# Kernel tuning notes

Measured on AMD Instinct MI355X. Metric: run time of the kernel, lower is better.

The kernel has to match this reference:

```python
import jax, jax.numpy as jnp
import numpy as np

HEADS, KV_HEADS, HEAD_DIM = 16, 4, 128
WINDOW, ROPE_THETA, EPS = 512, 10000.0, 1e-6


def _rms_norm(x, w):
    # Gemma RMSNorm: float32 compute, scale = 1 + w
    xf = x.astype(jnp.float32)
    y = xf * jax.lax.rsqrt(jnp.mean(xf * xf, axis=-1, keepdims=True) + EPS)
    return (y * (1.0 + w.astype(jnp.float32))).astype(x.dtype)


def _rope_cos_sin(T, dtype):
    inv_freq = 1.0 / ROPE_THETA ** (jnp.arange(0, HEAD_DIM, 2, dtype=jnp.float32) / HEAD_DIM)
    pos = jnp.arange(T, dtype=jnp.float32)
    freqs = pos[:, None] * inv_freq[None, :]          # [T, Dh/2]
    emb = jnp.concatenate([freqs, freqs], axis=-1)    # [T, Dh]
    return emb.astype(dtype), emb  # cos/sin applied below


def _rotate_half(x):
    x1, x2 = jnp.split(x, 2, axis=-1)
    return jnp.concatenate([-x2, x1], axis=-1)


def setup_inputs() -> dict:
    key = jax.random.key(0)
    ks = jax.random.split(key, 7)
    B, T, D = 2, 2048, 2048
    s = lambda k, shape, fan: jax.random.normal(k, shape, jnp.float32) * (fan ** -0.5)
    return {
        "x": jax.random.normal(ks[0], (B, T, D), jnp.float32),
        "Wq": s(ks[1], (HEADS * HEAD_DIM, D), D),
        "Wk": s(ks[2], (KV_HEADS * HEAD_DIM, D), D),
        "Wv": s(ks[3], (KV_HEADS * HEAD_DIM, D), D),
        "Wo": s(ks[4], (D, HEADS * HEAD_DIM), HEADS * HEAD_DIM),
        "qn_w": jax.random.normal(ks[5], (HEAD_DIM,), jnp.float32) * 0.02,
        "kn_w": jax.random.normal(ks[6], (HEAD_DIM,), jnp.float32) * 0.02,
    }


def reference(x, Wq, Wk, Wv, Wo, qn_w, kn_w):
    B, T, D = x.shape
    H, Hkv, Dh = HEADS, KV_HEADS, HEAD_DIM
    G = H // Hkv

    q = (x @ Wq.T).reshape(B, T, H, Dh).transpose(0, 2, 1, 3)     # [B,H,T,Dh]
    k = (x @ Wk.T).reshape(B, T, Hkv, Dh).transpose(0, 2, 1, 3)   # [B,Hkv,T,Dh]
    v = (x @ Wv.T).reshape(B, T, Hkv, Dh).transpose(0, 2, 1, 3)

    q = _rms_norm(q, qn_w)
    k = _rms_norm(k, kn_w)

    emb_c, emb_f = _rope_cos_sin(T, x.dtype)
    cos = jnp.cos(emb_f).astype(x.dtype)[None, None]  # [1,1,T,Dh]
    sin = jnp.sin(emb_f).astype(x.dtype)[None, None]
    q = q * cos + _rotate_half(q) * sin
    k = k * cos + _rotate_half(k) * sin

    q = q * (Dh ** -0.5)
    qg = q.reshape(B, Hkv, G, T, Dh)

    scores = jnp.einsum('bhgtd,bhkd->bhgtk', qg.astype(jnp.float32), k.astype(jnp.float32))

    dist = jnp.arange(T)[:, None] - jnp.arange(T)[None, :]        # [T,T]
    mask = (dist >= 0) & (dist <= WINDOW)
    scores = jnp.where(mask[None, None, None], scores, jnp.finfo(jnp.float32).min)
    att = jax.nn.softmax(scores, axis=-1).astype(x.dtype)

    ctx = jnp.einsum('bhgtk,bhkd->bhgtd', att, v)                 # [B,Hkv,G,T,Dh]
    out = ctx.reshape(B, H, T, Dh).transpose(0, 2, 1, 3).reshape(B, T, H * Dh)
    return out @ Wo.T
```

## Files before the change

### kernel.cpp

```cpp
#include <hip/hip_runtime.h>
#include <stdint.h>


typedef __attribute__((ext_vector_type(8))) short bf16x8;
typedef __attribute__((ext_vector_type(4))) float f32x4;

typedef __attribute__((address_space(3))) unsigned int lds_u32;
typedef const __attribute__((address_space(1))) unsigned int glb_u32;

__device__ __forceinline__ unsigned short f2bf(float f) {
  unsigned int x = __builtin_bit_cast(unsigned int, f);
  x += 0x7FFFu + ((x >> 16) & 1u);
  return (unsigned short)(x >> 16);
}

__global__ __launch_bounds__(256) void castall(const float* __restrict__ x,
                                               const float* __restrict__ wq,
                                               const float* __restrict__ wk,
                                               const float* __restrict__ wv,
                                               const float* __restrict__ wo,
                                               unsigned short* __restrict__ xb,
                                               unsigned short* __restrict__ wqkvb,
                                               unsigned short* __restrict__ wob) {
  int i = blockIdx.x * 256 + threadIdx.x;
  const float* src;
  unsigned short* dst;
  int off;
  if (i < 2097152)       { src = x;  dst = xb;              off = i; }
  else if (i < 3145728)  { src = wq; dst = wqkvb;           off = i - 2097152; }
  else if (i < 3407872)  { src = wk; dst = wqkvb + 4194304; off = i - 3145728; }
  else if (i < 3670016)  { src = wv; dst = wqkvb + 5242880; off = i - 3407872; }
  else                   { src = wo; dst = wob;             off = i - 3670016; }
  float4 v = ((const float4*)src)[off];
  uint2 o;
  o.x = (unsigned)f2bf(v.x) | ((unsigned)f2bf(v.y) << 16);
  o.y = (unsigned)f2bf(v.z) | ((unsigned)f2bf(v.w) << 16);
  ((uint2*)dst)[off] = o;
}

__global__ __launch_bounds__(256) void rope_tab(float* __restrict__ c,
                                                float* __restrict__ s) {
  int idx = blockIdx.x * 256 + threadIdx.x;
  int t = idx >> 6, i = idx & 63;
  float invf = exp2f(-(float)i * (13.287712379549449f / 64.0f));
  float a = (float)t * invf;
  c[idx] = cosf(a);
  s[idx] = sinf(a);
}

template <int BN>
__global__ __launch_bounds__(512, 2) void gemm256(const unsigned short* __restrict__ A,
                                                  const unsigned short* __restrict__ Bm,
                                                  float* __restrict__ C,
                                                  int N, int K) {
  constexpr int BSL = BN * 128;
  __shared__ uint8_t lds[65536 + 2 * BSL];
  const int tid = threadIdx.x, lane = tid & 63, w = tid >> 6;
  const int wm = w >> 2, wn = w & 3;
  const size_t m0 = (size_t)blockIdx.y * 256, n0 = (size_t)blockIdx.x * BN;
  const int srow = lane >> 3;
  const int schunk = (lane & 7) ^ srow;

  f32x4 acc[8][BN / 64];
#pragma unroll
  for (int i = 0; i < 8; ++i)
#pragma unroll
    for (int j = 0; j < BN / 64; ++j) acc[i][j] = f32x4{0.f, 0.f, 0.f, 0.f};

  const int NT = K >> 6;

  auto stageA = [&](int t, int par) {
    uint8_t* slot = lds + (par << 15);
#pragma unroll
    for (int j = 0; j < 4; ++j) {
      int r0 = (j * 8 + w) * 8;
      const unsigned short* src =
          A + (m0 + r0 + srow) * (size_t)K + t * 64 + schunk * 8;
      __builtin_amdgcn_global_load_lds((glb_u32*)src,
                                       (lds_u32*)(slot + r0 * 128), 16, 0, 0);
    }
  };
  auto stageB = [&](int t, int par) {
    uint8_t* slot = lds + 65536 + par * BSL;
#pragma unroll
    for (int j = 0; j < BN / 64; ++j) {
      int r0 = (j * 8 + w) * 8;
      const unsigned short* src =
          Bm + (n0 + r0 + srow) * (size_t)K + t * 64 + schunk * 8;
      __builtin_amdgcn_global_load_lds((glb_u32*)src,
                                       (lds_u32*)(slot + r0 * 128), 16, 0, 0);
    }
  };
  auto compute = [&](int par, int h) {
    const uint8_t* Asl = lds + (par << 15);
    const uint8_t* Bsl = lds + 65536 + par * BSL;
    bf16x8 af[8], bf[BN / 64];
    const int x7 = lane & 7;
    const int cx = h * 4 + (lane >> 4);
    const int rab = wm * 128 + (lane & 15);
    const int rbb = wn * (BN / 4) + (lane & 15);
#pragma unroll
    for (int mt = 0; mt < 8; ++mt)
      af[mt] = *(const bf16x8*)(Asl + (rab + mt * 16) * 128 + ((cx ^ x7) << 4));
#pragma unroll
    for (int nt = 0; nt < BN / 64; ++nt)
      bf[nt] = *(const bf16x8*)(Bsl + (rbb + nt * 16) * 128 + ((cx ^ x7) << 4));
    __builtin_amdgcn_s_setprio(1);
#pragma unroll
    for (int mt = 0; mt < 8; ++mt)
#pragma unroll
      for (int nt = 0; nt < BN / 64; ++nt)
        acc[mt][nt] = __builtin_amdgcn_mfma_f32_16x16x32_bf16(
            af[mt], bf[nt], acc[mt][nt], 0, 0, 0);
    __builtin_amdgcn_s_setprio(0);
  };

  stageA(0, 0);
  stageB(0, 0);
  for (int t = 0; t < NT - 1; ++t) {
    const int p = t & 1, q = p ^ 1;
    stageA(t + 1, q);
    asm volatile("s_waitcnt vmcnt(4)" ::: "memory");
    __builtin_amdgcn_s_barrier();
    __builtin_amdgcn_sched_barrier(0);
    compute(p, 0);
    stageB(t + 1, q);
    compute(p, 1);
    asm volatile("" ::: "memory");
    __builtin_amdgcn_s_barrier();
    __builtin_amdgcn_sched_barrier(0);
  }
  {
    const int p = (NT - 1) & 1;
    asm volatile("s_waitcnt vmcnt(0)" ::: "memory");
    __builtin_amdgcn_s_barrier();
    __builtin_amdgcn_sched_barrier(0);
    compute(p, 0);
    compute(p, 1);
  }
#pragma unroll
  for (int mt = 0; mt < 8; ++mt)
#pragma unroll
    for (int nt = 0; nt < BN / 64; ++nt) {
      size_t row = m0 + wm * 128 + mt * 16 + (lane >> 4) * 4;
      size_t col = n0 + wn * (BN / 4) + nt * 16 + (lane & 15);
#pragma unroll
      for (int r = 0; r < 4; ++r)
        C[(row + r) * N + col] = acc[mt][nt][r];
    }
}

__global__ __launch_bounds__(256) void eplg(const float* __restrict__ qkv,
                                            const float* __restrict__ qw,
                                            const float* __restrict__ kw,
                                            const float* __restrict__ rc,
                                            const float* __restrict__ rs,
                                            unsigned short* __restrict__ qb,
                                            unsigned short* __restrict__ kb) {
  const int row = blockIdx.x;
  const int t = row & 2047;
  const int lane = threadIdx.x & 63, w = threadIdx.x >> 6;
  const float* base = qkv + (size_t)row * 3072;
  const int d0 = 2 * lane;
  const float c0 = rc[t * 64 + (d0 & 63)];
  const float c1 = rc[t * 64 + ((d0 + 1) & 63)];
  const float s0 = rs[t * 64 + (d0 & 63)];
  const float s1 = rs[t * 64 + ((d0 + 1) & 63)];
  const float sgn = (lane < 32) ? -1.0f : 1.0f;
  const float QS = 0.12751744817f;

#pragma unroll
  for (int hh = 0; hh < 4; ++hh) {
    int h = w * 4 + hh;
    float2 x = *(const float2*)(base + h * 128 + d0);
    float ss = x.x * x.x + x.y * x.y;
#pragma unroll
    for (int m = 1; m < 64; m <<= 1) ss += __shfl_xor(ss, m);
    float r = rsqrtf(ss * (1.0f / 128.0f) + 1e-6f);
    float y0 = x.x * r * (1.0f + qw[d0]);
    float y1 = x.y * r * (1.0f + qw[d0 + 1]);
    float p0 = __shfl_xor(y0, 32);
    float p1 = __shfl_xor(y1, 32);
    float o0 = (y0 * c0 + sgn * p0 * s0) * QS;
    float o1 = (y1 * c1 + sgn * p1 * s1) * QS;
    unsigned int pk = (unsigned)f2bf(o0) | ((unsigned)f2bf(o1) << 16);
    *(unsigned int*)(qb + (size_t)row * 2048 + h * 128 + d0) = pk;
  }
  {
    float2 x = *(const float2*)(base + 2048 + w * 128 + d0);
    float ss = x.x * x.x + x.y * x.y;
#pragma unroll
    for (int m = 1; m < 64; m <<= 1) ss += __shfl_xor(ss, m);
    float r = rsqrtf(ss * (1.0f / 128.0f) + 1e-6f);
    float y0 = x.x * r * (1.0f + kw[d0]);
    float y1 = x.y * r * (1.0f + kw[d0 + 1]);
    float p0 = __shfl_xor(y0, 32);
    float p1 = __shfl_xor(y1, 32);
    float o0 = y0 * c0 + sgn * p0 * s0;
    float o1 = y1 * c1 + sgn * p1 * s1;
    unsigned int pk = (unsigned)f2bf(o0) | ((unsigned)f2bf(o1) << 16);
    *(unsigned int*)(kb + (size_t)row * 512 + w * 128 + d0) = pk;
  }
}

__global__ __launch_bounds__(256) void vtrans(const float* __restrict__ qkvf,
                                              unsigned short* __restrict__ vbt) {
  __shared__ float tile[64][65];
  const int t0 = blockIdx.x * 64;
  const int d0 = blockIdx.y * 64;
  const int b = blockIdx.z;
  const int tid = threadIdx.x;
#pragma unroll
  for (int i = 0; i < 4; ++i) {
    int idx = tid + 256 * i;
    int r = idx >> 4, c4 = idx & 15;
    float4 v = *(const float4*)(qkvf + (size_t)(b * 2048 + t0 + r) * 3072 +
                                2560 + d0 + c4 * 4);
    tile[r][c4 * 4 + 0] = v.x;
    tile[r][c4 * 4 + 1] = v.y;
    tile[r][c4 * 4 + 2] = v.z;
    tile[r][c4 * 4 + 3] = v.w;
  }
  __syncthreads();
  const int dr = tid >> 2, ts = (tid & 3) * 16;
  unsigned short tmp[16];
#pragma unroll
  for (int j = 0; j < 16; ++j) tmp[j] = f2bf(tile[ts + j][dr]);
  uint4* dst = (uint4*)(vbt + (size_t)(b * 512 + d0 + dr) * 2048 + t0 + ts);
  dst[0] = *(uint4*)(tmp);
  dst[1] = *(uint4*)(tmp + 8);
}

__global__ __launch_bounds__(1024) void attn(const unsigned short* __restrict__ qb,
                                             const unsigned short* __restrict__ kb,
                                             const unsigned short* __restrict__ vbt,
                                             unsigned short* __restrict__ ctxb) {
  __shared__ uint8_t Ks[2][64 * 256];
  __shared__ uint8_t Vs[2][128 * 128];
  __shared__ uint8_t Ps[16][16 * 128];
  const int qi = blockIdx.x, kvh = blockIdx.y, b = blockIdx.z;
  const int t0 = qi * 64;
  const int tid = threadIdx.x, lane = tid & 63, w = tid >> 6;
  const int h = kvh * 4 + (w & 3), wq = w >> 2;

  bf16x8 qf[4];
  {
    int qrow = t0 + wq * 16 + (lane & 15);
    const unsigned short* qp =
        qb + (size_t)(b * 2048 + qrow) * 2048 + h * 128 + (lane >> 4) * 8;
#pragma unroll
    for (int kc = 0; kc < 4; ++kc) qf[kc] = *(const bf16x8*)(qp + kc * 32);
  }
  f32x4 of[8];
#pragma unroll
  for (int i = 0; i < 8; ++i) of[i] = f32x4{0.f, 0.f, 0.f, 0.f};
  float m_run[4], l_run[4];
#pragma unroll
  for (int r = 0; r < 4; ++r) { m_run[r] = -1e30f; l_run[r] = 0.0f; }

  int kt0 = t0 - 512; if (kt0 < 0) kt0 = 0;
  const int nt = (t0 + 64 - kt0) >> 6;
  uint8_t* Pw = Ps[w];

  const int krow_s = 4 * w + (lane >> 4);
  const int kchunk_s = (lane & 15) ^ (krow_s & 7);
  const int vrow_s = 8 * w + (lane >> 3);
  const int vchunk_s = (lane & 7) ^ (vrow_s & 7);
  auto stage = [&](int it, int par) {
    int kt = kt0 + (it << 6);
    const unsigned short* ksrc =
        kb + (size_t)(b * 2048 + kt + krow_s) * 512 + kvh * 128 + kchunk_s * 8;
    __builtin_amdgcn_global_load_lds((glb_u32*)ksrc,
                                     (lds_u32*)(&Ks[par][w * 1024]), 16, 0, 0);
    const unsigned short* vsrc =
        vbt + (size_t)(b * 512 + kvh * 128 + vrow_s) * 2048 + kt + vchunk_s * 8;
    __builtin_amdgcn_global_load_lds((glb_u32*)vsrc,
                                     (lds_u32*)(&Vs[par][w * 1024]), 16, 0, 0);
  };

  stage(0, 0);
  for (int it = 0; it < nt; ++it) {
    const int par = it & 1;
    const int kt = kt0 + (it << 6);
    if (it + 1 < nt) {
      stage(it + 1, par ^ 1);
      asm volatile("s_waitcnt vmcnt(2)" ::: "memory");
    } else {
      asm volatile("s_waitcnt vmcnt(0)" ::: "memory");
    }
    __builtin_amdgcn_s_barrier();
    __builtin_amdgcn_sched_barrier(0);

    f32x4 sf[4];
#pragma unroll
    for (int nc = 0; nc < 4; ++nc) {
      f32x4 s = f32x4{0.f, 0.f, 0.f, 0.f};
      int key = nc * 16 + (lane & 15);
#pragma unroll
      for (int kc = 0; kc < 4; ++kc) {
        bf16x8 kf = *(const bf16x8*)(
            Ks[par] + key * 256 + (((lane >> 4) * 16 + kc * 64) ^ ((key & 7) << 4)));
        s = __builtin_amdgcn_mfma_f32_16x16x32_bf16(qf[kc], kf, s, 0, 0, 0);
      }
      sf[nc] = s;
    }
#pragma unroll
    for (int nc = 0; nc < 4; ++nc) {
      int j = kt + nc * 16 + (lane & 15);
#pragma unroll
      for (int r = 0; r < 4; ++r) {
        int tq = t0 + wq * 16 + (lane >> 4) * 4 + r;
        if (!((j <= tq) && (tq - j <= 512))) sf[nc][r] = -1e30f;
      }
    }
    float mx[4];
#pragma unroll
    for (int r = 0; r < 4; ++r) {
      float m = fmaxf(fmaxf(sf[0][r], sf[1][r]), fmaxf(sf[2][r], sf[3][r]));
      m = fmaxf(m, __shfl_xor(m, 1));
      m = fmaxf(m, __shfl_xor(m, 2));
      m = fmaxf(m, __shfl_xor(m, 4));
      m = fmaxf(m, __shfl_xor(m, 8));
      mx[r] = m;
    }
    bool grow = (mx[0] > m_run[0] + 8.0f) | (mx[1] > m_run[1] + 8.0f) |
                (mx[2] > m_run[2] + 8.0f) | (mx[3] > m_run[3] + 8.0f);
    if (__any(grow)) {
      float alpha[4];
#pragma unroll
      for (int r = 0; r < 4; ++r) {
        float mn = fmaxf(m_run[r], mx[r]);
        alpha[r] = exp2f(m_run[r] - mn);
        m_run[r] = mn;
        l_run[r] *= alpha[r];
      }
#pragma unroll
      for (int i = 0; i < 8; ++i)
#pragma unroll
        for (int r = 0; r < 4; ++r) of[i][r] *= alpha[r];
    }
    float l_add[4] = {0.f, 0.f, 0.f, 0.f};
#pragma unroll
    for (int nc = 0; nc < 4; ++nc)
#pragma unroll
      for (int r = 0; r < 4; ++r) {
        float p = exp2f(sf[nc][r] - m_run[r]);
        sf[nc][r] = p;
        l_add[r] += p;
      }
#pragma unroll
    for (int r = 0; r < 4; ++r) {
      float la = l_add[r];
      la += __shfl_xor(la, 1);
      la += __shfl_xor(la, 2);
      la += __shfl_xor(la, 4);
      la += __shfl_xor(la, 8);
      l_run[r] += la;
    }
#pragma unroll
    for (int nc = 0; nc < 4; ++nc) {
      int key = nc * 16 + (lane & 15);
#pragma unroll
      for (int r = 0; r < 4; ++r) {
        int prow = (lane >> 4) * 4 + r;
        *(unsigned short*)(Pw + prow * 128 + ((key * 2) ^ ((prow & 7) << 4))) =
            f2bf(sf[nc][r]);
      }
    }
#pragma unroll
    for (int ks = 0; ks < 2; ++ks) {
      int prow = lane & 15;
      bf16x8 pf = *(const bf16x8*)(
          Pw + prow * 128 + ((ks * 64 + (lane >> 4) * 16) ^ ((prow & 7) << 4)));
#pragma unroll
      for (int nc8 = 0; nc8 < 8; ++nc8) {
        int vrow = nc8 * 16 + (lane & 15);
        bf16x8 vf = *(const bf16x8*)(
            Vs[par] + vrow * 128 + ((ks * 64 + (lane >> 4) * 16) ^ ((vrow & 7) << 4)));
        of[nc8] = __builtin_amdgcn_mfma_f32_16x16x32_bf16(pf, vf, of[nc8], 0, 0, 0);
      }
    }
    asm volatile("" ::: "memory");
    __builtin_amdgcn_s_barrier();
    __builtin_amdgcn_sched_barrier(0);
  }
#pragma unroll
  for (int nc8 = 0; nc8 < 8; ++nc8)
#pragma unroll
    for (int r = 0; r < 4; ++r) {
      int tq = t0 + wq * 16 + (lane >> 4) * 4 + r;
      int col = h * 128 + nc8 * 16 + (lane & 15);
      ctxb[(size_t)(b * 2048 + tq) * 2048 + col] = f2bf(of[nc8][r] / l_run[r]);
    }
}

extern "C" void kernel_launch(void* const* d_in, const int* in_sizes, int n_in,
                              void* d_out, int out_size, void* d_ws, size_t ws_size,
                              hipStream_t stream) {
  const float* x  = (const float*)d_in[0];
  const float* Wq = (const float*)d_in[1];
  const float* Wk = (const float*)d_in[2];
  const float* Wv = (const float*)d_in[3];
  const float* Wo = (const float*)d_in[4];
  const float* qw = (const float*)d_in[5];
  const float* kw = (const float*)d_in[6];

  uint8_t* ws = (uint8_t*)d_ws;
  if (ws_size < 131072000ull) return;
  unsigned short* xb    = (unsigned short*)(ws);
  unsigned short* wqkvb = (unsigned short*)(ws + 16777216);
  unsigned short* wob   = (unsigned short*)(ws + 29360128);
  float*          qkvf  = (float*)(ws + 37748736);
  unsigned short* qb2   = (unsigned short*)(ws + 88080384);
  unsigned short* kb2   = (unsigned short*)(ws + 104857600);
  unsigned short* vbt   = (unsigned short*)(ws + 109051904);
  unsigned short* ctxb  = (unsigned short*)(ws + 113246208);
  float*          ropec = (float*)(ws + 130023424);
  float*          ropes = (float*)(ws + 130547712);

  castall<<<18432, 256, 0, stream>>>(x, Wq, Wk, Wv, Wo, xb, wqkvb, wob);
  rope_tab<<<512, 256, 0, stream>>>(ropec, ropes);
  {
    dim3 g(3072 / 256, 4096 / 256);
    gemm256<256><<<g, 512, 0, stream>>>(xb, wqkvb, qkvf, 3072, 2048);
  }
  eplg<<<4096, 256, 0, stream>>>(qkvf, qw, kw, ropec, ropes, qb2, kb2);
  {
    dim3 g(32, 8, 2);
    vtrans<<<g, 256, 0, stream>>>(qkvf, vbt);
  }
  {
    dim3 g(32, 4, 2);
    attn<<<g, 1024, 0, stream>>>(qb2, kb2, vbt, ctxb);
  }
  {
    dim3 g(2048 / 128, 4096 / 256);
    gemm256<128><<<g, 512, 0, stream>>>(ctxb, wob, (float*)d_out, 2048, 2048);
  }
}
```

Baseline: 285.6 us.

## Add ping-pong pipelined 256x256 GEMM for QKV projection with split-K LDS stages

Adds a new bf16 MFMA GEMM kernel for the QKV projection that splits each 64-wide K tile into two 32-wide LDS slots. It stages loads for upcoming tiles with global_load_lds while computing the current half-tiles, interleaving barriers and raised wave priority around MFMA bursts. It also uses a different LDS swizzle. The aim is to overlap global memory traffic with matrix math and keep the MFMA units busier. The cost is a 128 KB LDS footprint and many barriers per iteration, which may limit occupancy, and the schedule relies on hand-tuned vmcnt counts.

Measured after the change: 285.7 us. Within noise of the previous version (+0.0%).

```diff
diff --git a/kernel.cpp b/kernel.cpp
--- a/kernel.cpp
+++ b/kernel.cpp
@@ -48,6 +48,142 @@
   s[idx] = sinf(a);
 }
 
+__global__ __launch_bounds__(512, 2) void gemm8p(const unsigned short* __restrict__ A,
+                                                 const unsigned short* __restrict__ Bm,
+                                                 float* __restrict__ C,
+                                                 int N, int K) {
+  __shared__ uint8_t lds[131072];
+  const int tid = threadIdx.x, lane = tid & 63, w = tid >> 6;
+  const int wm = w >> 2, wn = w & 3;
+  const size_t m0 = (size_t)blockIdx.y * 256, n0 = (size_t)blockIdx.x * 256;
+  const int s_rl = lane >> 2;
+  const int s_c  = ((lane & 3) + 4 - ((lane >> 3) & 3)) & 3;
+
+  f32x4 acc[8][4];
+#pragma unroll
+  for (int i = 0; i < 8; ++i)
+#pragma unroll
+    for (int j = 0; j < 4; ++j) acc[i][j] = f32x4{0.f, 0.f, 0.f, 0.f};
+
+  auto slot = [&](int par, int op, int ks) -> uint8_t* {
+    return lds + (((par * 2 + op) * 2 + ks) << 14);
+  };
+  auto stage = [&](const unsigned short* P, size_t row0, int t, int ks,
+                   uint8_t* sl) {
+#pragma unroll
+    for (int j = 0; j < 2; ++j) {
+      int seg = j * 8 + w;
+      const unsigned short* src =
+          P + (row0 + seg * 16 + s_rl) * (size_t)K + t * 64 + ks * 32 + s_c * 8;
+      __builtin_amdgcn_global_load_lds((glb_u32*)src,
+                                       (lds_u32*)(sl + seg * 1024), 16, 0, 0);
+    }
+  };
+  auto readA = [&](int par, int ks, int qm, bf16x8* out) {
+    const uint8_t* sl = slot(par, 0, ks);
+#pragma unroll
+    for (int mt = 0; mt < 4; ++mt) {
+      int r = wm * 128 + qm * 64 + mt * 16 + (lane & 15);
+      int c = lane >> 4;
+      out[mt] = *(const bf16x8*)(sl + r * 64 + (((c + ((r >> 1) & 3)) & 3) << 4));
+    }
+  };
+  auto readB = [&](int par, int ks, bf16x8* out) {
+    const uint8_t* sl = slot(par, 1, ks);
+#pragma unroll
+    for (int nt = 0; nt < 4; ++nt) {
+      int r = wn * 64 + nt * 16 + (lane & 15);
+      int c = lane >> 4;
+      out[nt] = *(const bf16x8*)(sl + r * 64 + (((c + ((r >> 1) & 3)) & 3) << 4));
+    }
+  };
+  auto mfma16 = [&](int qm, const bf16x8* a, const bf16x8* b) {
+    __builtin_amdgcn_s_setprio(1);
+#pragma unroll
+    for (int mt = 0; mt < 4; ++mt)
+#pragma unroll
+      for (int nt = 0; nt < 4; ++nt)
+        acc[qm * 4 + mt][nt] = __builtin_amdgcn_mfma_f32_16x16x32_bf16(
+            a[mt], b[nt], acc[qm * 4 + mt][nt], 0, 0, 0);
+    __builtin_amdgcn_s_setprio(0);
+  };
+
+#define BAR()  __builtin_amdgcn_s_barrier(); __builtin_amdgcn_sched_barrier(0)
+#define LGKM0() asm volatile("s_waitcnt lgkmcnt(0)" ::: "memory"); \
+                __builtin_amdgcn_sched_barrier(0)
+
+  const int ITERS = K >> 7;
+  stage(A, m0, 0, 0, slot(0, 0, 0));
+  stage(Bm, n0, 0, 0, slot(0, 1, 0));
+  stage(A, m0, 0, 1, slot(0, 0, 1));
+  stage(Bm, n0, 0, 1, slot(0, 1, 1));
+  stage(A, m0, 1, 0, slot(1, 0, 0));
+  stage(Bm, n0, 1, 0, slot(1, 1, 0));
+  asm volatile("s_waitcnt vmcnt(4)" ::: "memory");
+  BAR();
+
+  bf16x8 a[4], bq[4];
+  for (int i = 0; i < ITERS; ++i) {
+    const int t1 = 2 * i + 1, t2 = 2 * i + 2, t3 = 2 * i + 3;
+    const bool more = (i + 1 < ITERS);
+    readB(0, 0, bq); readA(0, 0, 0, a);
+    stage(A, m0, t1, 1, slot(1, 0, 1));
+    BAR(); LGKM0();
+    mfma16(0, a, bq);
+    BAR();
+    readA(0, 0, 1, a);
+    stage(Bm, n0, t1, 1, slot(1, 1, 1));
+    BAR(); LGKM0();
+    mfma16(1, a, bq);
+    BAR();
+    readB(0, 1, bq); readA(0, 1, 0, a);
+    if (more) stage(A, m0, t2, 0, slot(0, 0, 0));
+    BAR(); LGKM0();
+    mfma16(0, a, bq);
+    BAR();
+    readA(0, 1, 1, a);
+    if (more) stage(Bm, n0, t2, 0, slot(0, 1, 0));
+    BAR(); LGKM0();
+    mfma16(1, a, bq);
+    if (more) { asm volatile("s_waitcnt vmcnt(4)" ::: "memory"); }
+    else      { asm volatile("s_waitcnt vmcnt(0)" ::: "memory"); }
+    BAR();
+    readB(1, 0, bq); readA(1, 0, 0, a);
+    if (more) stage(A, m0, t2, 1, slot(0, 0, 1));
+    BAR(); LGKM0();
+    mfma16(0, a, bq);
+    BAR();
+    readA(1, 0, 1, a);
+    if (more) stage(Bm, n0, t2, 1, slot(0, 1, 1));
+    BAR(); LGKM0();
+    mfma16(1, a, bq);
+    BAR();
+    readB(1, 1, bq); readA(1, 1, 0, a);
+    if (more) stage(A, m0, t3, 0, slot(1, 0, 0));
+    BAR(); LGKM0();
+    mfma16(0, a, bq);
+    BAR();
+    readA(1, 1, 1, a);
+    if (more) stage(Bm, n0, t3, 0, slot(1, 1, 0));
+    BAR(); LGKM0();
+    mfma16(1, a, bq);
+    if (more) { asm volatile("s_waitcnt vmcnt(4)" ::: "memory"); }
+    BAR();
+  }
+#undef BAR
+#undef LGKM0
+#pragma unroll
+  for (int mt = 0; mt < 8; ++mt)
+#pragma unroll
+    for (int nt = 0; nt < 4; ++nt) {
+      size_t row = m0 + wm * 128 + mt * 16 + (lane >> 4) * 4;
+      size_t col = n0 + wn * 64 + nt * 16 + (lane & 15);
+#pragma unroll
+      for (int r = 0; r < 4; ++r)
+        C[(row + r) * N + col] = acc[mt][nt][r];
+    }
+}
+
 template <int BN>
 __global__ __launch_bounds__(512, 2) void gemm256(const unsigned short* __restrict__ A,
                                                   const unsigned short* __restrict__ Bm,
@@ -422,7 +558,7 @@
   rope_tab<<<512, 256, 0, stream>>>(ropec, ropes);
   {
     dim3 g(3072 / 256, 4096 / 256);
-    gemm256<256><<<g, 512, 0, stream>>>(xb, wqkvb, qkvf, 3072, 2048);
+    gemm8p<<<g, 512, 0, stream>>>(xb, wqkvb, qkvf, 3072, 2048);
   }
   eplg<<<4096, 256, 0, stream>>>(qkvf, qw, kw, ropec, ropes, qb2, kb2);
   {
```
